# Optimization experiments

Measured on AMD Instinct MI355X. Metric: run time of the kernel, lower is better.

Reference implementation:

```python
import jax, jax.numpy as jnp
import numpy as np

GAMMA = 0.05


def _sq_dists(a, b):
    # squared euclidean pairwise distances: ||a||^2 + ||b||^2 - 2 a.b
    aa = jnp.sum(a * a, axis=1)[:, None]
    bb = jnp.sum(b * b, axis=1)[None, :]
    d2 = aa + bb - 2.0 * jnp.matmul(a, b.T)
    return jnp.maximum(d2, 0.0)


def _rbf(a, b, gamma):
    return jnp.exp(-gamma * _sq_dists(a, b))


def setup_inputs() -> dict:
    key = jax.random.key(0)
    k1, k2, k3 = jax.random.split(key, 3)
    n, m, d = 8192, 8192, 128
    N = jax.random.normal(k1, (n, d), dtype=jnp.float32)
    R = jax.random.normal(k2, (m, d), dtype=jnp.float32)
    weights = jax.random.uniform(k3, (n, 1), dtype=jnp.float32)
    return {"N": N, "R": R, "weights": weights}


def reference(N, R, weights):
    w = jnp.squeeze(weights / jnp.sum(weights))  # [n]
    m = R.shape[0]
    w_y = jnp.ones((m,), dtype=R.dtype) / m      # [m]
    # x-x term: weighted sum of RBF kernel over N x N
    xx = jnp.sum((w[:, None] * w[None, :]) * _rbf(N, N, GAMMA))
    # y-y term: plain mean over R x R
    yy = jnp.mean(_rbf(R, R, GAMMA))
    # x-y term: weights outer uniform weights
    xy = jnp.sum((w[:, None] * w_y[None, :]) * _rbf(N, R, GAMMA))
    mmd = xx + yy - 2.0 * xy
    return jnp.sqrt(mmd)
```

## Files before the change

kernel.cpp:

```cpp
#include <hip/hip_runtime.h>
#include <hip/hip_bf16.h>
#include <math.h>

#define GAMMA 0.05f
#define NP 32
#define SYM 528

typedef __attribute__((ext_vector_type(8))) short bf16x8;
typedef __attribute__((ext_vector_type(4))) float f32x4;

static __device__ __forceinline__ unsigned f32_to_bf16(float x) {
    unsigned u = __float_as_uint(x);
    u += 0x7fffu + ((u >> 16) & 1u);
    return u >> 16;
}

static __device__ __forceinline__ void gload_lds16(const void* g, void* l) {
    __builtin_amdgcn_global_load_lds(
        (const __attribute__((address_space(1))) void*)g,
        (__attribute__((address_space(3))) void*)l, 16, 0, 0);
}


__global__ __launch_bounds__(256) void prep_kernel(
    const float* __restrict__ Nmat, const float* __restrict__ Rmat,
    const float* __restrict__ W,
    float* __restrict__ ENw, float* __restrict__ ER,
    unsigned short* __restrict__ Nsw, unsigned short* __restrict__ Rsw,
    int nblkN)
{
    const int isR  = (blockIdx.x >= nblkN) ? 1 : 0;
    const int bloc = blockIdx.x - isR * nblkN;
    const int wrp  = threadIdx.x >> 6;
    const int lane = threadIdx.x & 63;
    const int row  = bloc * 4 + wrp;

    const float* X = isR ? Rmat : Nmat;
    unsigned short* Xsw = isR ? Rsw : Nsw;

    float2 v = *(const float2*)(X + (size_t)row * 128 + lane * 2);
    float s = fmaf(v.x, v.x, v.y * v.y);
    unsigned hbits = f32_to_bf16(v.x) | (f32_to_bf16(v.y) << 16);

    const int kb = lane * 4;
    const int hf = kb >> 7;
    const int koff = (kb & 127) ^ ((row & 7) << 4);
    size_t off = ((size_t)(row >> 8) << 16) + ((size_t)hf << 15)
               + ((size_t)(row & 255) << 7) + koff;
    *(unsigned*)((char*)Xsw + off) = hbits;

    #pragma unroll
    for (int o = 32; o > 0; o >>= 1) s += __shfl_down(s, o);

    if (lane == 0) {
        float e = __expf(-GAMMA * s);
        if (!isR) ENw[row] = W[row] * e;
        else      ER[row]  = e;
    }
}

__global__ __launch_bounds__(512, 2) void mmd_mfma_kernel(
    const unsigned short* __restrict__ Nsw, const unsigned short* __restrict__ Rsw,
    const float* __restrict__ ENw, const float* __restrict__ ER,
    double* __restrict__ acc3)
{
    int mode, bi, bj;
    {
        int bid = blockIdx.x;
        if (bid < 2 * SYM) {
            mode = (bid >= SYM) ? 1 : 0;
            int t = bid - mode * SYM;
            int i = (int)(32.5f - sqrtf(1056.25f - 2.0f * (float)t));
            if (i < 0) i = 0;
            while ((i + 1) * NP - ((i + 1) * i) / 2 <= t) ++i;
            while (i * NP - (i * (i - 1)) / 2 > t) --i;
            bi = i;
            bj = i + (t - (i * NP - (i * (i - 1)) / 2));
        } else {
            mode = 2;
            int t = bid - 2 * SYM;
            bi = t >> 5;
            bj = t & 31;
        }
    }

    const unsigned short *A, *B; const float *EA, *EB;
    if (mode == 0)      { A = Nsw; B = Nsw; EA = ENw; EB = ENw; }
    else if (mode == 1) { A = Rsw; B = Rsw; EA = ER;  EB = ER;  }
    else                { A = Nsw; B = Rsw; EA = ENw; EB = ER;  }

    const float scale = (mode < 2 && bj > bi) ? 2.0f : 1.0f;
    const bool diagblk = (mode < 2 && bi == bj);

    __shared__ __align__(16) char lds[131072];
    __shared__ double red[8];

    const int tid  = threadIdx.x;
    const int lane = tid & 63;
    const int wv   = tid >> 6;

    const char* gA = (const char*)A + ((size_t)bi << 16);
    const char* gB = (const char*)B + ((size_t)bj << 16);

    #pragma unroll
    for (int it = 0; it < 4; ++it) {
        int c = (wv * 4 + it) * 1024;
        gload_lds16(gA + c + lane * 16, lds + c);
        gload_lds16(gB + c + lane * 16, lds + 65536 + c);
    }
    __builtin_amdgcn_sched_barrier(0);
    #pragma unroll
    for (int it = 0; it < 4; ++it) {
        int c = (wv * 4 + it) * 1024;
        gload_lds16(gA + 32768 + c + lane * 16, lds + 32768 + c);
        gload_lds16(gB + 32768 + c + lane * 16, lds + 98304 + c);
    }
    __builtin_amdgcn_sched_barrier(0);
    asm volatile("s_waitcnt vmcnt(8)" ::: "memory");
    __builtin_amdgcn_s_barrier();
    __builtin_amdgcn_sched_barrier(0);

    const int wm = wv >> 2;
    const int wn = wv & 3;
    const int lg = lane >> 4;
    const int lr = lane & 15;
    const int swz = (lr & 7) << 4;

    f32x4 acc[8][4];
    #pragma unroll
    for (int mi = 0; mi < 8; ++mi)
        #pragma unroll
        for (int nj = 0; nj < 4; ++nj) acc[mi][nj] = (f32x4){0.f,0.f,0.f,0.f};

    #define DO_KS(ks)                                                          \
    {                                                                          \
        const int hb   = ((ks) >> 1) * 32768;                                  \
        const int koff = ((((ks) & 1) * 64 + lg * 16) ^ swz);                  \
        bf16x8 af[8], bfr[4];                                                  \
        _Pragma("unroll")                                                      \
        for (int mi = 0; mi < 8; ++mi) {                                       \
            int r = wm * 128 + mi * 16 + lr;                                   \
            af[mi] = *(const bf16x8*)(lds + hb + r * 128 + koff);              \
        }                                                                      \
        _Pragma("unroll")                                                      \
        for (int nj = 0; nj < 4; ++nj) {                                       \
            int r = wn * 64 + nj * 16 + lr;                                    \
            bfr[nj] = *(const bf16x8*)(lds + 65536 + hb + r * 128 + koff);     \
        }                                                                      \
        __builtin_amdgcn_s_setprio(1);                                         \
        _Pragma("unroll")                                                      \
        for (int mi = 0; mi < 8; ++mi)                                         \
            _Pragma("unroll")                                                  \
            for (int nj = 0; nj < 4; ++nj)                                     \
                acc[mi][nj] = __builtin_amdgcn_mfma_f32_16x16x32_bf16(         \
                    af[mi], bfr[nj], acc[mi][nj], 0, 0, 0);                    \
        __builtin_amdgcn_s_setprio(0);                                         \
    }

    DO_KS(0)
    DO_KS(1)
    asm volatile("s_waitcnt vmcnt(0)" ::: "memory");
    __builtin_amdgcn_s_barrier();
    __builtin_amdgcn_sched_barrier(0);
    DO_KS(2)
    DO_KS(3)
    #undef DO_KS

    float eb[4];
    #pragma unroll
    for (int nj = 0; nj < 4; ++nj) eb[nj] = EB[bj * 256 + wn * 64 + nj * 16 + lr];

    float part = 0.f;
    if (!diagblk) {
        #pragma unroll
        for (int mi = 0; mi < 8; ++mi) {
            float4 ea4 = *(const float4*)&EA[bi * 256 + wm * 128 + mi * 16 + lg * 4];
            #pragma unroll
            for (int r = 0; r < 4; ++r) {
                float rowsum = 0.f;
                #pragma unroll
                for (int nj = 0; nj < 4; ++nj)
                    rowsum = fmaf(eb[nj], __expf(2.0f * GAMMA * acc[mi][nj][r]), rowsum);
                part = fmaf(((const float*)&ea4)[r], rowsum, part);
            }
        }
    } else {
        #pragma unroll
        for (int mi = 0; mi < 8; ++mi) {
            float4 ea4 = *(const float4*)&EA[bi * 256 + wm * 128 + mi * 16 + lg * 4];
            #pragma unroll
            for (int r = 0; r < 4; ++r) {
                int ci = wm * 128 + mi * 16 + lg * 4 + r;
                float rowsum = 0.f;
                #pragma unroll
                for (int nj = 0; nj < 4; ++nj) {
                    float e = __expf(2.0f * GAMMA * acc[mi][nj][r]);
                    if (ci == wn * 64 + nj * 16 + lr) e = 0.f;
                    rowsum = fmaf(eb[nj], e, rowsum);
                }
                part = fmaf(((const float*)&ea4)[r], rowsum, part);
            }
        }
    }
    part *= scale;

    double dp = (double)part;
    #pragma unroll
    for (int o = 32; o > 0; o >>= 1) dp += __shfl_down(dp, o);
    if (lane == 0) red[wv] = dp;
    __syncthreads();
    if (tid == 0) {
        double t = 0.0;
        #pragma unroll
        for (int i = 0; i < 8; ++i) t += red[i];
        atomicAdd(&acc3[mode], t);
    }
}

__global__ __launch_bounds__(256) void finalize_kernel(const float* __restrict__ W,
                                                       const double* __restrict__ acc,
                                                       float* __restrict__ out,
                                                       int n, int m) {
    __shared__ double redS[256], redS2[256];
    double s = 0.0, s2 = 0.0;
    for (int i = threadIdx.x; i < n; i += 256) {
        double w = (double)W[i];
        s += w; s2 += w * w;
    }
    redS[threadIdx.x] = s; redS2[threadIdx.x] = s2;
    __syncthreads();
    for (int stride = 128; stride > 0; stride >>= 1) {
        if (threadIdx.x < stride) {
            redS[threadIdx.x]  += redS[threadIdx.x + stride];
            redS2[threadIdx.x] += redS2[threadIdx.x + stride];
        }
        __syncthreads();
    }
    if (threadIdx.x == 0) {
        double S = redS[0], S2 = redS2[0];
        double xx = (acc[0] + S2) / (S * S);
        double yy = (acc[1] + (double)m) / ((double)m * (double)m);
        double xy = acc[2] / (S * (double)m);
        out[0] = (float)sqrt(fmax(xx + yy - 2.0 * xy, 0.0));
    }
}

extern "C" void kernel_launch(void* const* d_in, const int* in_sizes, int n_in,
                              void* d_out, int out_size, void* d_ws, size_t ws_size,
                              hipStream_t stream) {
    const float* Nmat = (const float*)d_in[0];
    const float* Rmat = (const float*)d_in[1];
    const float* W    = (const float*)d_in[2];
    float* out = (float*)d_out;

    const int n = in_sizes[2];
    const int d = in_sizes[0] / n;
    const int m = in_sizes[1] / d;

    double* acc         = (double*)d_ws;
    float* ENw          = (float*)((char*)d_ws + 1024);
    float* ER           = (float*)((char*)d_ws + 33792);
    unsigned short* Nsw = (unsigned short*)((char*)d_ws + 66560);
    unsigned short* Rsw = (unsigned short*)((char*)d_ws + 66560 + 2097152);

    hipMemsetAsync(d_ws, 0, 64, stream);

    prep_kernel<<<(n + m) / 4, 256, 0, stream>>>(Nmat, Rmat, W, ENw, ER, Nsw, Rsw, n / 4);

    mmd_mfma_kernel<<<2 * SYM + NP * NP, 512, 0, stream>>>(Nsw, Rsw, ENw, ER, acc);

    finalize_kernel<<<1, 256, 0, stream>>>(W, acc, out, n, m);
}
```

Baseline: 134.6 us.

## Shrink MFMA tiles to 128x128, fuse finalize via last-block counter, drop memset

Halves the output tile per block from 256x256 to 128x128 with 256 threads and a simpler row-major swizzled layout, loading the full K dimension at once. This raises the block count from 2080 to 8256 for better load balance and occupancy, at the cost of more global/L2 traffic per FLOP. It also removes the memset and finalize kernel launches by zeroing accumulators in the prep kernel and having the last-finishing block compute the final result via an atomic counter.

```diff
diff --git a/kernel.cpp b/kernel.cpp
--- a/kernel.cpp
+++ b/kernel.cpp
@@ -3,8 +3,9 @@
 #include <math.h>
 
 #define GAMMA 0.05f
-#define NP 32
-#define SYM 528
+#define NP2 64
+#define SYM2 2080
+#define NBLK 8256
 
 typedef __attribute__((ext_vector_type(8))) short bf16x8;
 typedef __attribute__((ext_vector_type(4))) float f32x4;
@@ -27,8 +28,10 @@
     const float* __restrict__ W,
     float* __restrict__ ENw, float* __restrict__ ER,
     unsigned short* __restrict__ Nsw, unsigned short* __restrict__ Rsw,
-    int nblkN)
+    unsigned* __restrict__ zero_region, int nblkN)
 {
+    if (blockIdx.x == 0 && threadIdx.x < 17) zero_region[threadIdx.x] = 0u;
+
     const int isR  = (blockIdx.x >= nblkN) ? 1 : 0;
     const int bloc = blockIdx.x - isR * nblkN;
     const int wrp  = threadIdx.x >> 6;
@@ -42,12 +45,8 @@
     float s = fmaf(v.x, v.x, v.y * v.y);
     unsigned hbits = f32_to_bf16(v.x) | (f32_to_bf16(v.y) << 16);
 
-    const int kb = lane * 4;
-    const int hf = kb >> 7;
-    const int koff = (kb & 127) ^ ((row & 7) << 4);
-    size_t off = ((size_t)(row >> 8) << 16) + ((size_t)hf << 15)
-               + ((size_t)(row & 255) << 7) + koff;
-    *(unsigned*)((char*)Xsw + off) = hbits;
+    int boff = (lane * 4) ^ ((row & 7) << 4);
+    *(unsigned*)((char*)Xsw + (size_t)row * 256 + boff) = hbits;
 
     #pragma unroll
     for (int o = 32; o > 0; o >>= 1) s += __shfl_down(s, o);
@@ -59,28 +58,30 @@
     }
 }
 
-__global__ __launch_bounds__(512, 2) void mmd_mfma_kernel(
+__global__ __launch_bounds__(256, 2) void mmd_mfma_kernel(
     const unsigned short* __restrict__ Nsw, const unsigned short* __restrict__ Rsw,
     const float* __restrict__ ENw, const float* __restrict__ ER,
-    double* __restrict__ acc3)
+    const float* __restrict__ W,
+    double* __restrict__ acc3, unsigned* __restrict__ counter,
+    float* __restrict__ out)
 {
     int mode, bi, bj;
     {
         int bid = blockIdx.x;
-        if (bid < 2 * SYM) {
-            mode = (bid >= SYM) ? 1 : 0;
-            int t = bid - mode * SYM;
-            int i = (int)(32.5f - sqrtf(1056.25f - 2.0f * (float)t));
+        if (bid < 2 * SYM2) {
+            mode = (bid >= SYM2) ? 1 : 0;
+            int t = bid - mode * SYM2;
+            int i = (int)(64.5f - sqrtf(4160.25f - 2.0f * (float)t));
             if (i < 0) i = 0;
-            while ((i + 1) * NP - ((i + 1) * i) / 2 <= t) ++i;
-            while (i * NP - (i * (i - 1)) / 2 > t) --i;
+            while ((i + 1) * NP2 - ((i + 1) * i) / 2 <= t) ++i;
+            while (i * NP2 - (i * (i - 1)) / 2 > t) --i;
             bi = i;
-            bj = i + (t - (i * NP - (i * (i - 1)) / 2));
+            bj = i + (t - (i * NP2 - (i * (i - 1)) / 2));
         } else {
             mode = 2;
-            int t = bid - 2 * SYM;
-            bi = t >> 5;
-            bj = t & 31;
+            int t = bid - 2 * SYM2;
+            bi = t >> 6;
+            bj = t & 63;
         }
     }
 
@@ -92,89 +93,70 @@
     const float scale = (mode < 2 && bj > bi) ? 2.0f : 1.0f;
     const bool diagblk = (mode < 2 && bi == bj);
 
-    __shared__ __align__(16) char lds[131072];
-    __shared__ double red[8];
+    __shared__ __align__(16) char lds[65536];
+    __shared__ double red[4];
+    __shared__ int is_last;
 
     const int tid  = threadIdx.x;
     const int lane = tid & 63;
     const int wv   = tid >> 6;
 
-    const char* gA = (const char*)A + ((size_t)bi << 16);
-    const char* gB = (const char*)B + ((size_t)bj << 16);
-
-    #pragma unroll
-    for (int it = 0; it < 4; ++it) {
-        int c = (wv * 4 + it) * 1024;
+    const char* gA = (const char*)A + ((size_t)bi << 15);
+    const char* gB = (const char*)B + ((size_t)bj << 15);
+
+    #pragma unroll
+    for (int it = 0; it < 8; ++it) {
+        int c = (wv * 8 + it) * 1024;
         gload_lds16(gA + c + lane * 16, lds + c);
-        gload_lds16(gB + c + lane * 16, lds + 65536 + c);
-    }
-    __builtin_amdgcn_sched_barrier(0);
-    #pragma unroll
-    for (int it = 0; it < 4; ++it) {
-        int c = (wv * 4 + it) * 1024;
-        gload_lds16(gA + 32768 + c + lane * 16, lds + 32768 + c);
-        gload_lds16(gB + 32768 + c + lane * 16, lds + 98304 + c);
-    }
-    __builtin_amdgcn_sched_barrier(0);
-    asm volatile("s_waitcnt vmcnt(8)" ::: "memory");
-    __builtin_amdgcn_s_barrier();
-    __builtin_amdgcn_sched_barrier(0);
-
-    const int wm = wv >> 2;
-    const int wn = wv & 3;
+        gload_lds16(gB + c + lane * 16, lds + 32768 + c);
+    }
+    __syncthreads();
+
+    const int wm = wv >> 1;
+    const int wn = wv & 1;
     const int lg = lane >> 4;
     const int lr = lane & 15;
     const int swz = (lr & 7) << 4;
 
-    f32x4 acc[8][4];
-    #pragma unroll
-    for (int mi = 0; mi < 8; ++mi)
+    f32x4 acc[4][4];
+    #pragma unroll
+    for (int mi = 0; mi < 4; ++mi)
         #pragma unroll
         for (int nj = 0; nj < 4; ++nj) acc[mi][nj] = (f32x4){0.f,0.f,0.f,0.f};
 
-    #define DO_KS(ks)                                                          \
-    {                                                                          \
-        const int hb   = ((ks) >> 1) * 32768;                                  \
-        const int koff = ((((ks) & 1) * 64 + lg * 16) ^ swz);                  \
-        bf16x8 af[8], bfr[4];                                                  \
-        _Pragma("unroll")                                                      \
-        for (int mi = 0; mi < 8; ++mi) {                                       \
-            int r = wm * 128 + mi * 16 + lr;                                   \
-            af[mi] = *(const bf16x8*)(lds + hb + r * 128 + koff);              \
-        }                                                                      \
-        _Pragma("unroll")                                                      \
-        for (int nj = 0; nj < 4; ++nj) {                                       \
-            int r = wn * 64 + nj * 16 + lr;                                    \
-            bfr[nj] = *(const bf16x8*)(lds + 65536 + hb + r * 128 + koff);     \
-        }                                                                      \
-        __builtin_amdgcn_s_setprio(1);                                         \
-        _Pragma("unroll")                                                      \
-        for (int mi = 0; mi < 8; ++mi)                                         \
-            _Pragma("unroll")                                                  \
-            for (int nj = 0; nj < 4; ++nj)                                     \
-                acc[mi][nj] = __builtin_amdgcn_mfma_f32_16x16x32_bf16(         \
-                    af[mi], bfr[nj], acc[mi][nj], 0, 0, 0);                    \
-        __builtin_amdgcn_s_setprio(0);                                         \
-    }
-
-    DO_KS(0)
-    DO_KS(1)
-    asm volatile("s_waitcnt vmcnt(0)" ::: "memory");
-    __builtin_amdgcn_s_barrier();
-    __builtin_amdgcn_sched_barrier(0);
-    DO_KS(2)
-    DO_KS(3)
-    #undef DO_KS
+    #pragma unroll
+    for (int ks = 0; ks < 4; ++ks) {
+        const int koff = (ks * 64 + lg * 16) ^ swz;
+        bf16x8 af[4], bfr[4];
+        #pragma unroll
+        for (int mi = 0; mi < 4; ++mi) {
+            int r = wm * 64 + mi * 16 + lr;
+            af[mi] = *(const bf16x8*)(lds + r * 256 + koff);
+        }
+        #pragma unroll
+        for (int nj = 0; nj < 4; ++nj) {
+            int r = wn * 64 + nj * 16 + lr;
+            bfr[nj] = *(const bf16x8*)(lds + 32768 + r * 256 + koff);
+        }
+        __builtin_amdgcn_s_setprio(1);
+        #pragma unroll
+        for (int mi = 0; mi < 4; ++mi)
+            #pragma unroll
+            for (int nj = 0; nj < 4; ++nj)
+                acc[mi][nj] = __builtin_amdgcn_mfma_f32_16x16x32_bf16(
+                    af[mi], bfr[nj], acc[mi][nj], 0, 0, 0);
+        __builtin_amdgcn_s_setprio(0);
+    }
 
     float eb[4];
     #pragma unroll
-    for (int nj = 0; nj < 4; ++nj) eb[nj] = EB[bj * 256 + wn * 64 + nj * 16 + lr];
+    for (int nj = 0; nj < 4; ++nj) eb[nj] = EB[bj * 128 + wn * 64 + nj * 16 + lr];
 
     float part = 0.f;
     if (!diagblk) {
         #pragma unroll
-        for (int mi = 0; mi < 8; ++mi) {
-            float4 ea4 = *(const float4*)&EA[bi * 256 + wm * 128 + mi * 16 + lg * 4];
+        for (int mi = 0; mi < 4; ++mi) {
+            float4 ea4 = *(const float4*)&EA[bi * 128 + wm * 64 + mi * 16 + lg * 4];
             #pragma unroll
             for (int r = 0; r < 4; ++r) {
                 float rowsum = 0.f;
@@ -186,11 +168,11 @@
         }
     } else {
         #pragma unroll
-        for (int mi = 0; mi < 8; ++mi) {
-            float4 ea4 = *(const float4*)&EA[bi * 256 + wm * 128 + mi * 16 + lg * 4];
+        for (int mi = 0; mi < 4; ++mi) {
+            float4 ea4 = *(const float4*)&EA[bi * 128 + wm * 64 + mi * 16 + lg * 4];
             #pragma unroll
             for (int r = 0; r < 4; ++r) {
-                int ci = wm * 128 + mi * 16 + lg * 4 + r;
+                int ci = wm * 64 + mi * 16 + lg * 4 + r;
                 float rowsum = 0.f;
                 #pragma unroll
                 for (int nj = 0; nj < 4; ++nj) {
@@ -210,38 +192,41 @@
     if (lane == 0) red[wv] = dp;
     __syncthreads();
     if (tid == 0) {
-        double t = 0.0;
-        #pragma unroll
-        for (int i = 0; i < 8; ++i) t += red[i];
-        atomicAdd(&acc3[mode], t);
-    }
-}
-
-__global__ __launch_bounds__(256) void finalize_kernel(const float* __restrict__ W,
-                                                       const double* __restrict__ acc,
-                                                       float* __restrict__ out,
-                                                       int n, int m) {
-    __shared__ double redS[256], redS2[256];
-    double s = 0.0, s2 = 0.0;
-    for (int i = threadIdx.x; i < n; i += 256) {
-        double w = (double)W[i];
-        s += w; s2 += w * w;
-    }
-    redS[threadIdx.x] = s; redS2[threadIdx.x] = s2;
+        atomicAdd(&acc3[mode], red[0] + red[1] + red[2] + red[3]);
+        __threadfence();
+        unsigned old = atomicAdd(counter, 1u);
+        is_last = (old == NBLK - 1) ? 1 : 0;
+    }
     __syncthreads();
-    for (int stride = 128; stride > 0; stride >>= 1) {
-        if (threadIdx.x < stride) {
-            redS[threadIdx.x]  += redS[threadIdx.x + stride];
-            redS2[threadIdx.x] += redS2[threadIdx.x + stride];
-        }
+
+    if (is_last) {
+        double s = 0.0, s2 = 0.0;
+        for (int i = tid; i < 8192; i += 256) {
+            double w = (double)W[i];
+            s += w; s2 += w * w;
+        }
+        double* redS  = (double*)lds;
+        double* redS2 = (double*)lds + 256;
+        redS[tid] = s; redS2[tid] = s2;
         __syncthreads();
-    }
-    if (threadIdx.x == 0) {
-        double S = redS[0], S2 = redS2[0];
-        double xx = (acc[0] + S2) / (S * S);
-        double yy = (acc[1] + (double)m) / ((double)m * (double)m);
-        double xy = acc[2] / (S * (double)m);
-        out[0] = (float)sqrt(fmax(xx + yy - 2.0 * xy, 0.0));
+        for (int stride = 128; stride > 0; stride >>= 1) {
+            if (tid < stride) {
+                redS[tid]  += redS[tid + stride];
+                redS2[tid] += redS2[tid + stride];
+            }
+            __syncthreads();
+        }
+        if (tid == 0) {
+            double S = redS[0], S2 = redS2[0];
+            double xxo = atomicAdd(&acc3[0], 0.0);
+            double yyo = atomicAdd(&acc3[1], 0.0);
+            double xyv = atomicAdd(&acc3[2], 0.0);
+            double M = 8192.0;
+            double xx = (xxo + S2) / (S * S);
+            double yy = (yyo + M) / (M * M);
+            double xy = xyv / (S * M);
+            out[0] = (float)sqrt(fmax(xx + yy - 2.0 * xy, 0.0));
+        }
     }
 }
 
@@ -258,16 +243,14 @@
     const int m = in_sizes[1] / d;
 
     double* acc         = (double*)d_ws;
+    unsigned* counter   = (unsigned*)((char*)d_ws + 64);
     float* ENw          = (float*)((char*)d_ws + 1024);
     float* ER           = (float*)((char*)d_ws + 33792);
     unsigned short* Nsw = (unsigned short*)((char*)d_ws + 66560);
     unsigned short* Rsw = (unsigned short*)((char*)d_ws + 66560 + 2097152);
 
-    hipMemsetAsync(d_ws, 0, 64, stream);
-
-    prep_kernel<<<(n + m) / 4, 256, 0, stream>>>(Nmat, Rmat, W, ENw, ER, Nsw, Rsw, n / 4);
-
-    mmd_mfma_kernel<<<2 * SYM + NP * NP, 512, 0, stream>>>(Nsw, Rsw, ENw, ER, acc);
-
-    finalize_kernel<<<1, 256, 0, stream>>>(W, acc, out, n, m);
-}
+    prep_kernel<<<(n + m) / 4, 256, 0, stream>>>(Nmat, Rmat, W, ENw, ER, Nsw, Rsw,
+                                                 (unsigned*)d_ws, n / 4);
+
+    mmd_mfma_kernel<<<NBLK, 256, 0, stream>>>(Nsw, Rsw, ENw, ER, W, acc, counter, out);
+}
```

New measurement: 243.3 us. +80.8%, slower.
